# Kernel tuning notes

Measured on AMD Instinct MI355X. Metric: run time of the kernel, lower is better.

## Reference

```python
import jax, jax.numpy as jnp
import numpy as np

B, N, E, D, H, M, NH, T = 32, 128, 16256, 64, 128, 128, 256, 2

def setup_inputs() -> dict:
    key = jax.random.key(0)
    ks = jax.random.split(key, 20)
    inp = {
        'inputs': jax.random.normal(ks[0], (B, N, D), jnp.float32),
        'rel_rec': jax.random.uniform(ks[1], (E, N), jnp.float32),
        'rel_send': jax.random.uniform(ks[2], (E, N), jnp.float32),
        'rel_type': jax.random.uniform(ks[3], (B, E, T), jnp.float32),
        'indices': jnp.arange(E, dtype=jnp.int64 if jax.config.jax_enable_x64 else jnp.int32).reshape(2, E // 2),
        # per-edge-type MLP weights (torch Linear: w [out,in], b [out])
        'msg_fc1_w': jax.random.normal(ks[4], (T, H, D), jnp.float32) * 0.05,
        'msg_fc1_b': jax.random.normal(ks[5], (T, H), jnp.float32) * 0.05,
        'msg_fc2_w': jax.random.normal(ks[6], (T, M, H), jnp.float32) * 0.05,
        'msg_fc2_b': jax.random.normal(ks[7], (T, M), jnp.float32) * 0.05,
        'msg_fc3_w': jax.random.normal(ks[8], (T, H, D), jnp.float32) * 0.05,
        'msg_fc3_b': jax.random.normal(ks[9], (T, H), jnp.float32) * 0.05,
        'msg_fc4_w': jax.random.normal(ks[10], (T, M, H), jnp.float32) * 0.05,
        'msg_fc4_b': jax.random.normal(ks[11], (T, M), jnp.float32) * 0.05,
        'out_fc1_w': jax.random.normal(ks[12], (NH, M), jnp.float32) * 0.05,
        'out_fc1_b': jax.random.normal(ks[13], (NH,), jnp.float32) * 0.05,
        'out_fc2_w': jax.random.normal(ks[14], (NH, NH), jnp.float32) * 0.05,
        'out_fc2_b': jax.random.normal(ks[15], (NH,), jnp.float32) * 0.05,
        'out_fc3_w': jax.random.normal(ks[16], (D, NH), jnp.float32) * 0.05,
        'out_fc3_b': jax.random.normal(ks[17], (D,), jnp.float32) * 0.05,
    }
    return inp

def _linear(x, w, b):
    return jnp.einsum('bed,od->beo', x, w) + b

def reference(inputs, rel_rec, rel_send, rel_type, indices,
              msg_fc1_w, msg_fc1_b, msg_fc2_w, msg_fc2_b,
              msg_fc3_w, msg_fc3_b, msg_fc4_w, msg_fc4_b,
              out_fc1_w, out_fc1_b, out_fc2_w, out_fc2_b, out_fc3_w, out_fc3_b):
    # pre_msg: [B, E, D]
    pre_msg = jnp.einsum('en,bnd->bed', rel_send, inputs)
    idx_s, idx_a = indices[0], indices[1]  # disjoint edge-id partitions
    all_msgs = jnp.zeros((pre_msg.shape[0], pre_msg.shape[1], M), pre_msg.dtype)
    pm_s = pre_msg[:, idx_s, :]  # [B, E/2, D]
    pm_a = pre_msg[:, idx_a, :]
    for i in range(T):  # small fixed edge-type loop (dropout p=0 -> no-op)
        m_s = jax.nn.relu(_linear(jax.nn.relu(_linear(pm_s, msg_fc1_w[i], msg_fc1_b[i])), msg_fc2_w[i], msg_fc2_b[i]))
        m_s = m_s * rel_type[:, idx_s, i:i + 1]
        all_msgs = all_msgs.at[:, idx_s, :].add(m_s)
        m_a = jax.nn.relu(_linear(jax.nn.relu(_linear(pm_a, msg_fc3_w[i], msg_fc3_b[i])), msg_fc4_w[i], msg_fc4_b[i]))
        m_a = m_a * rel_type[:, idx_a, i:i + 1]
        all_msgs = all_msgs.at[:, idx_a, :].add(m_a)
    # aggregate: [B, N, M]
    agg = jnp.einsum('bem,en->bnm', all_msgs, rel_rec)
    h = jax.nn.relu(jnp.einsum('bnm,om->bno', agg, out_fc1_w) + out_fc1_b)
    h = jax.nn.relu(jnp.einsum('bnh,oh->bno', h, out_fc2_w) + out_fc2_b)
    pred = jnp.einsum('bnh,oh->bno', h, out_fc3_w) + out_fc3_b
    return inputs + pred
```

## Files before the change

kernel.cpp:

```cpp
#include <hip/hip_runtime.h>
#include <hip/hip_bf16.h>

#define NB 32
#define NN 128
#define NE 16256
#define ND 64
#define NHID 128
#define NM 128
#define NOH 256
#define NT 2
#define EHALF 8128
#define NTILE 127
#define TILE_E 64

typedef short s16x8 __attribute__((ext_vector_type(8)));
typedef short s16x4 __attribute__((ext_vector_type(4)));
typedef float f32x4 __attribute__((ext_vector_type(4)));

#define MFMA16(a, b, c) __builtin_amdgcn_mfma_f32_16x16x32_bf16((a), (b), (c), 0, 0, 0)

#define PARTIAL_SZ ((size_t)256 * 128 * 128 * 2)
#define WS_RS      (PARTIAL_SZ)
#define RS_SZ      ((size_t)NE * 128 * 2)
#define WS_RRT     (WS_RS + RS_SZ)
#define RRT_SZ     ((size_t)128 * NE * 2)
#define WS_IWA     (WS_RRT + RRT_SZ)
#define IWA_SZ     ((size_t)NB * 2 * 2 * 128 * 128 * 2)
#define WS_OW      (WS_IWA + IWA_SZ)
#define OW_SZ      ((size_t)(32768 + 65536 + 16384) * 2)

__device__ __forceinline__ ushort f2bf(float x) {
    uint u = __float_as_uint(x);
    return (ushort)((u + 0x7fffu + ((u >> 16) & 1u)) >> 16);
}
__device__ __forceinline__ float bf2f(ushort h) {
    return __uint_as_float(((uint)h) << 16);
}
__device__ __forceinline__ float4 ldg4(const float* p) {
    return *reinterpret_cast<const float4*>(p);
}
__device__ __forceinline__ uint cvtpk(float lo, float hi) {
    uint r;
    asm("v_cvt_pk_bf16_f32 %0, %1, %2" : "=v"(r) : "v"(lo), "v"(hi));
    return r;
}
__device__ __forceinline__ char* swz16(void* base, int row, int bir) {
    return (char*)base + row * 256 + (bir ^ ((row & 15) << 4));
}
__device__ __forceinline__ const char* swz16c(const void* base, int row, int bir) {
    return (const char*)base + row * 256 + (bir ^ ((row & 15) << 4));
}
__device__ __forceinline__ char* swz8(void* base, int row, int bir) {
    return (char*)base + row * 128 + (bir ^ ((row & 7) << 4));
}
__device__ __forceinline__ const char* swz8c(const void* base, int row, int bir) {
    return (const char*)base + row * 128 + (bir ^ ((row & 7) << 4));
}
__device__ __forceinline__ char* swzR(void* base, int row, int rowBytes, int bir) {
    return (char*)base + row * rowBytes + (bir ^ ((row & 15) << 4));
}
__device__ __forceinline__ const char* swzRc(const void* base, int row, int rowBytes, int bir) {
    return (const char*)base + row * rowBytes + (bir ^ ((row & 15) << 4));
}
__device__ __forceinline__ void gload16(const void* g, void* l) {
    __builtin_amdgcn_global_load_lds(
        (const __attribute__((address_space(1))) void*)g,
        (__attribute__((address_space(3))) void*)l, 16, 0, 0);
}

__global__ __launch_bounds__(256)
void k_pre(const float* __restrict__ inputs,
           const float* __restrict__ rel_rec, const float* __restrict__ rel_send,
           const float* __restrict__ w1, const float* __restrict__ w3,
           const float* __restrict__ ow1, const float* __restrict__ ow2,
           const float* __restrict__ ow3,
           char* __restrict__ ws)
{
    ushort* rs  = (ushort*)(ws + WS_RS);
    ushort* rrT = (ushort*)(ws + WS_RRT);
    const int t = threadIdx.x;
    const int blk = blockIdx.x;
    __shared__ float lds[128][65];

    if (blk < 127) {
        const int eb = blk;
        for (int nh = 0; nh < 2; ++nh) {
            __syncthreads();
            for (int i = t; i < 128 * 64; i += 256) {
                int e = i >> 6, n = i & 63;
                lds[e][n] = rel_rec[(size_t)(eb * 128 + e) * 128 + nh * 64 + n];
            }
            __syncthreads();
            for (int i = t; i < 64 * 128; i += 256) {
                int n = i >> 7, e = i & 127;
                rrT[(size_t)(nh * 64 + n) * NE + eb * 128 + e] = f2bf(lds[e][n]);
            }
        }
    } else if (blk < 254) {
        const int eb = blk - 127;
        const float4* src = (const float4*)(rel_send + (size_t)eb * 16384);
        for (int i = t; i < 4096; i += 256) {
            float4 v = src[i];
            ushort4 o;
            o.x = f2bf(v.x); o.y = f2bf(v.y); o.z = f2bf(v.z); o.w = f2bf(v.w);
            *(ushort4*)(rs + (size_t)eb * 16384 + (size_t)i * 4) = o;
        }
    } else if (blk < 382) {
        ushort* iwa = (ushort*)(ws + WS_IWA);
        const int wg = blk - 254;
        const int b = wg >> 2, half = (wg >> 1) & 1, it = wg & 1;
        const float* WA  = (half ? w3 : w1) + (size_t)it * NHID * ND;
        const float* inp = inputs + (size_t)b * NN * ND;
        ushort* dst = iwa + (size_t)wg * NHID * NN;

        const int lane = t & 63, wave = t >> 6;
        const int l16 = lane & 15, l4 = lane >> 4;

        for (int hh = 0; hh < 2; ++hh) {
            const int ht = wave * 2 + hh;
            s16x8 bf[2];
#pragma unroll
            for (int ks = 0; ks < 2; ++ks) {
                const float* p = WA + (size_t)(ht * 16 + l16) * ND + ks * 32 + l4 * 8;
                float4 u = ldg4(p), v = ldg4(p + 4);
                s16x8 f;
                f[0] = (short)f2bf(u.x); f[1] = (short)f2bf(u.y);
                f[2] = (short)f2bf(u.z); f[3] = (short)f2bf(u.w);
                f[4] = (short)f2bf(v.x); f[5] = (short)f2bf(v.y);
                f[6] = (short)f2bf(v.z); f[7] = (short)f2bf(v.w);
                bf[ks] = f;
            }
            for (int nt = 0; nt < 8; ++nt) {
                s16x8 af[2];
#pragma unroll
                for (int ks = 0; ks < 2; ++ks) {
                    const float* p = inp + (size_t)(nt * 16 + l16) * ND + ks * 32 + l4 * 8;
                    float4 u = ldg4(p), v = ldg4(p + 4);
                    s16x8 f;
                    f[0] = (short)f2bf(u.x); f[1] = (short)f2bf(u.y);
                    f[2] = (short)f2bf(u.z); f[3] = (short)f2bf(u.w);
                    f[4] = (short)f2bf(v.x); f[5] = (short)f2bf(v.y);
                    f[6] = (short)f2bf(v.z); f[7] = (short)f2bf(v.w);
                    af[ks] = f;
                }
                f32x4 c = (f32x4){0.f, 0.f, 0.f, 0.f};
                c = MFMA16(af[0], bf[0], c);
                c = MFMA16(af[1], bf[1], c);
                s16x4 o;
                o[0] = (short)f2bf(c[0]); o[1] = (short)f2bf(c[1]);
                o[2] = (short)f2bf(c[2]); o[3] = (short)f2bf(c[3]);
                *(s16x4*)&dst[(size_t)(ht * 16 + l16) * NN + nt * 16 + l4 * 4] = o;
            }
        }
    } else {
        ushort* owbf = (ushort*)(ws + WS_OW);
        for (int i = t; i < 4096; i += 256) {
            const int ln = i & 63, ks = (i >> 6) & 3, ot = i >> 8;
            const float* src = ow1 + (size_t)(ot * 16 + (ln & 15)) * 128 + ks * 32 + (ln >> 4) * 8;
            ushort* d = owbf + (size_t)i * 8;
#pragma unroll
            for (int j = 0; j < 8; ++j) d[j] = f2bf(src[j]);
        }
        for (int i = t; i < 8192; i += 256) {
            const int ln = i & 63, ks = (i >> 6) & 7, ot = i >> 9;
            const float* src = ow2 + (size_t)(ot * 16 + (ln & 15)) * 256 + ks * 32 + (ln >> 4) * 8;
            ushort* d = owbf + 32768 + (size_t)i * 8;
#pragma unroll
            for (int j = 0; j < 8; ++j) d[j] = f2bf(src[j]);
        }
        for (int i = t; i < 2048; i += 256) {
            const int ln = i & 63, ks = (i >> 6) & 7, dt = i >> 9;
            const float* src = ow3 + (size_t)(dt * 16 + (ln & 15)) * 256 + ks * 32 + (ln >> 4) * 8;
            ushort* d = owbf + 98304 + (size_t)i * 8;
#pragma unroll
            for (int j = 0; j < 8; ++j) d[j] = f2bf(src[j]);
        }
    }
}

__global__ __launch_bounds__(512, 1)
void k_edge(const float* __restrict__ rel_type,
            const float* __restrict__ b1, const float* __restrict__ b2,
            const float* __restrict__ b3, const float* __restrict__ b4,
            const float* __restrict__ w2, const float* __restrict__ w4,
            char* __restrict__ ws)
{
    const ushort* rsg = (const ushort*)(ws + WS_RS);
    const ushort* rrT = (const ushort*)(ws + WS_RRT);
    const ushort* iwa = (const ushort*)(ws + WS_IWA);
    ushort* partial   = (ushort*)ws;

    const int tid  = threadIdx.x;
    const int wave = tid >> 6;
    const int lane = tid & 63;
    const int l16  = lane & 15;
    const int l4   = lane >> 4;

    const int wg    = blockIdx.x;
    const int b     = wg >> 3;
    const int half  = (wg >> 2) & 1;
    const int chunk = wg & 3;

    const float* BA    = half ? b3 : b1;
    const float* BB    = half ? b4 : b2;
    const float* WBsrc = half ? w4 : w2;

    __shared__ ushort H_s[2][2][64 * 128];
    __shared__ ushort rs_s[2][64 * 128];
    __shared__ ushort rr_s[2][128 * 64];
    __shared__ ushort Mt_s[128 * 64];
    __shared__ float  rt_s[2][128];

    s16x8 wIW[2][4];
    const ushort* iwb = iwa + (size_t)((b * 2 + half) * 2) * NHID * NN;
#pragma unroll
    for (int it = 0; it < 2; ++it)
#pragma unroll
        for (int ks = 0; ks < 4; ++ks)
            wIW[it][ks] = *(const s16x8*)(iwb + (size_t)it * NHID * NN +
                                          (size_t)(wave * 16 + l16) * NN + ks * 32 + l4 * 8);
    s16x8 wB[2][4];
#pragma unroll
    for (int it = 0; it < 2; ++it)
#pragma unroll
        for (int ks = 0; ks < 4; ++ks) {
            const float* p = WBsrc + (size_t)(it * NM + wave * 16 + l16) * NHID + ks * 32 + l4 * 8;
            float4 u = ldg4(p), v = ldg4(p + 4);
            s16x8 f;
            f[0] = (short)f2bf(u.x); f[1] = (short)f2bf(u.y);
            f[2] = (short)f2bf(u.z); f[3] = (short)f2bf(u.w);
            f[4] = (short)f2bf(v.x); f[5] = (short)f2bf(v.y);
            f[6] = (short)f2bf(v.z); f[7] = (short)f2bf(v.w);
            wB[it][ks] = f;
        }
    float biasA[2] = {BA[wave * 16 + l16], BA[NHID + wave * 16 + l16]};
    float biasB[2] = {BB[wave * 16 + l16], BB[NM + wave * 16 + l16]};

    f32x4 agg[8];
#pragma unroll
    for (int r = 0; r < 8; ++r) agg[r] = (f32x4){0.f, 0.f, 0.f, 0.f};

    const int t0 = chunk * 32;
    const int t1 = (t0 + 32 < NTILE) ? (t0 + 32) : NTILE;

    {
        const int ebase0 = half * EHALF + t0 * TILE_E;
#pragma unroll
        for (int s = 0; s < 2; ++s) {
            const int i = s * 512 + tid;
            const int e = i >> 4, c = i & 15;
            const int cp = c ^ (e & 15);
            gload16(rsg + (size_t)(ebase0 + e) * 128 + cp * 8, (char*)&rs_s[0][0] + i * 16);
        }
    }
    __syncthreads();

    for (int t = t0; t < t1; ++t) {
        const int buf  = (t - t0) & 1;
        const int nbuf = buf ^ 1;
        const int ebase = half * EHALF + t * TILE_E;
        const bool do_next = (t + 1) < t1;

#pragma unroll
        for (int s = 0; s < 2; ++s) {
            const int j = s * 512 + tid;
            const int n = j >> 3, c = j & 7;
            const int cp = c ^ (n & 7);
            gload16(rrT + (size_t)n * NE + ebase + cp * 8, (char*)&rr_s[buf][0] + j * 16);
        }
        if (do_next) {
            const int ebn = ebase + TILE_E;
#pragma unroll
            for (int s = 0; s < 2; ++s) {
                const int i = s * 512 + tid;
                const int e = i >> 4, c = i & 15;
                const int cp = c ^ (e & 15);
                gload16(rsg + (size_t)(ebn + e) * 128 + cp * 8, (char*)&rs_s[nbuf][0] + i * 16);
            }
        }
        if (tid < 128)
            rt_s[buf][tid] = rel_type[((size_t)b * NE + ebase + (tid >> 1)) * NT + (tid & 1)];

#pragma unroll
        for (int et = 0; et < 4; ++et) {
            const int erow = et * 16 + l16;
            s16x8 a0 = *(const s16x8*)swz16c(&rs_s[buf][0], erow, 0 * 64 + l4 * 16);
            s16x8 a1 = *(const s16x8*)swz16c(&rs_s[buf][0], erow, 1 * 64 + l4 * 16);
            s16x8 a2 = *(const s16x8*)swz16c(&rs_s[buf][0], erow, 2 * 64 + l4 * 16);
            s16x8 a3 = *(const s16x8*)swz16c(&rs_s[buf][0], erow, 3 * 64 + l4 * 16);
#pragma unroll
            for (int it = 0; it < 2; ++it) {
                f32x4 c = (f32x4){0.f, 0.f, 0.f, 0.f};
                __builtin_amdgcn_s_setprio(1);
                c = MFMA16(a0, wIW[it][0], c);
                c = MFMA16(a1, wIW[it][1], c);
                c = MFMA16(a2, wIW[it][2], c);
                c = MFMA16(a3, wIW[it][3], c);
                __builtin_amdgcn_s_setprio(0);
#pragma unroll
                for (int r = 0; r < 4; ++r) {
                    const int er = et * 16 + l4 * 4 + r;
                    *(ushort*)swz16(&H_s[buf][it][0], er, (wave * 16 + l16) * 2) =
                        f2bf(fmaxf(c[r] + biasA[it], 0.f));
                }
            }
        }
        __syncthreads();

        float macc[4][4];
#pragma unroll
        for (int et = 0; et < 4; ++et)
#pragma unroll
            for (int r = 0; r < 4; ++r) macc[et][r] = 0.f;

#pragma unroll
        for (int et = 0; et < 4; ++et) {
            const int e = et * 16 + l16;
            float2 rtv[4];
#pragma unroll
            for (int r = 0; r < 4; ++r)
                rtv[r] = *(const float2*)&rt_s[buf][(et * 16 + l4 * 4 + r) * 2];
#pragma unroll
            for (int it = 0; it < 2; ++it) {
                f32x4 c = (f32x4){0.f, 0.f, 0.f, 0.f};
                __builtin_amdgcn_s_setprio(1);
#pragma unroll
                for (int ks = 0; ks < 4; ++ks) {
                    s16x8 a = *(const s16x8*)swz16c(&H_s[buf][it][0], e, ks * 64 + l4 * 16);
                    c = MFMA16(a, wB[it][ks], c);
                }
                __builtin_amdgcn_s_setprio(0);
#pragma unroll
                for (int r = 0; r < 4; ++r)
                    macc[et][r] += fmaxf(c[r] + biasB[it], 0.f) * (it ? rtv[r].y : rtv[r].x);
            }
        }

        {
            const int m = wave * 16 + l16;
#pragma unroll
            for (int et = 0; et < 4; ++et) {
                uint2 v;
                v.x = cvtpk(macc[et][0], macc[et][1]);
                v.y = cvtpk(macc[et][2], macc[et][3]);
                *(uint2*)swz8(Mt_s, m, et * 32 + l4 * 8) = v;
            }
            s16x8 bb0 = *(const s16x8*)swz8c(Mt_s, m, 0 * 64 + l4 * 16);
            s16x8 bb1 = *(const s16x8*)swz8c(Mt_s, m, 1 * 64 + l4 * 16);
            __builtin_amdgcn_s_setprio(1);
#pragma unroll
            for (int nt = 0; nt < 8; ++nt) {
                const int n = nt * 16 + l16;
                s16x8 a0 = *(const s16x8*)swz8c(&rr_s[buf][0], n, 0 * 64 + l4 * 16);
                s16x8 a1 = *(const s16x8*)swz8c(&rr_s[buf][0], n, 1 * 64 + l4 * 16);
                agg[nt] = MFMA16(a0, bb0, agg[nt]);
                agg[nt] = MFMA16(a1, bb1, agg[nt]);
            }
            __builtin_amdgcn_s_setprio(0);
        }
    }

    {
        ushort* dst = partial + (size_t)wg * (NN * NM);
        const int m = wave * 16 + l16;
#pragma unroll
        for (int nt = 0; nt < 8; ++nt) {
            uint2 v;
            v.x = cvtpk(agg[nt][0], agg[nt][1]);
            v.y = cvtpk(agg[nt][2], agg[nt][3]);
            *(uint2*)&dst[(size_t)m * NN + nt * 16 + l4 * 4] = v;
        }
    }
}

__global__ __launch_bounds__(512)
void k_out(const ushort* __restrict__ partial,
           const ushort* __restrict__ owbf,
           const float* __restrict__ inputs,
           const float* __restrict__ ob1, const float* __restrict__ ob2,
           const float* __restrict__ ob3,
           float* __restrict__ out)
{
    const int t    = threadIdx.x;
    const int wave = t >> 6;
    const int lane = t & 63;
    const int l16  = lane & 15;
    const int l4   = lane >> 4;
    const int wg   = blockIdx.x;
    const int b    = wg >> 3;
    const int n0   = (wg & 7) * 16;

    __shared__ ushort xA[16 * 128];
    __shared__ ushort h1A[16 * 256];
    __shared__ ushort h2A[16 * 256];

    {
        const int m = t >> 2, g = t & 3;
        float s0 = 0.f, s1 = 0.f, s2 = 0.f, s3 = 0.f;
#pragma unroll
        for (int c = 0; c < 8; ++c) {
            const ushort* p = partial + ((size_t)(b * 8 + c)) * (NN * NM) +
                              (size_t)m * NN + n0 + g * 4;
            s16x4 v = *(const s16x4*)p;
            s0 += bf2f((ushort)v[0]); s1 += bf2f((ushort)v[1]);
            s2 += bf2f((ushort)v[2]); s3 += bf2f((ushort)v[3]);
        }
        *(ushort*)swzR(xA, g * 4 + 0, 256, m * 2) = f2bf(s0);
        *(ushort*)swzR(xA, g * 4 + 1, 256, m * 2) = f2bf(s1);
        *(ushort*)swzR(xA, g * 4 + 2, 256, m * 2) = f2bf(s2);
        *(ushort*)swzR(xA, g * 4 + 3, 256, m * 2) = f2bf(s3);
    }
    __syncthreads();

    {
        s16x8 ka[4];
#pragma unroll
        for (int ks = 0; ks < 4; ++ks)
            ka[ks] = *(const s16x8*)swzRc(xA, l16, 256, ks * 64 + l4 * 16);
#pragma unroll
        for (int ot = 0; ot < 2; ++ot) {
            const int otg = wave * 2 + ot;
            const int o = otg * 16 + l16;
            f32x4 c = (f32x4){0.f, 0.f, 0.f, 0.f};
#pragma unroll
            for (int ks = 0; ks < 4; ++ks) {
                s16x8 wb = *(const s16x8*)&owbf[((size_t)(otg * 4 + ks) * 64 + lane) * 8];
                c = MFMA16(ka[ks], wb, c);
            }
            const float bias = ob1[o];
#pragma unroll
            for (int r = 0; r < 4; ++r)
                *(ushort*)swzR(h1A, l4 * 4 + r, 512, o * 2) =
                    f2bf(fmaxf(c[r] + bias, 0.f));
        }
    }
    __syncthreads();

    {
        s16x8 ka[8];
#pragma unroll
        for (int ks = 0; ks < 8; ++ks)
            ka[ks] = *(const s16x8*)swzRc(h1A, l16, 512, ks * 64 + l4 * 16);
        const ushort* w2f = owbf + 32768;
#pragma unroll
        for (int ot = 0; ot < 2; ++ot) {
            const int otg = wave * 2 + ot;
            const int o = otg * 16 + l16;
            f32x4 c = (f32x4){0.f, 0.f, 0.f, 0.f};
#pragma unroll
            for (int ks = 0; ks < 8; ++ks) {
                s16x8 wb = *(const s16x8*)&w2f[((size_t)(otg * 8 + ks) * 64 + lane) * 8];
                c = MFMA16(ka[ks], wb, c);
            }
            const float bias = ob2[o];
#pragma unroll
            for (int r = 0; r < 4; ++r)
                *(ushort*)swzR(h2A, l4 * 4 + r, 512, o * 2) =
                    f2bf(fmaxf(c[r] + bias, 0.f));
        }
    }
    __syncthreads();

    if (wave < 4) {
        s16x8 ka[8];
#pragma unroll
        for (int ks = 0; ks < 8; ++ks)
            ka[ks] = *(const s16x8*)swzRc(h2A, l16, 512, ks * 64 + l4 * 16);
        const ushort* w3f = owbf + 98304;
        const int d = wave * 16 + l16;
        f32x4 c = (f32x4){0.f, 0.f, 0.f, 0.f};
#pragma unroll
        for (int ks = 0; ks < 8; ++ks) {
            s16x8 wb = *(const s16x8*)&w3f[((size_t)(wave * 8 + ks) * 64 + lane) * 8];
            c = MFMA16(ka[ks], wb, c);
        }
        const float bias = ob3[d];
#pragma unroll
        for (int r = 0; r < 4; ++r) {
            const int n = n0 + l4 * 4 + r;
            const size_t idx = ((size_t)b * NN + n) * ND + d;
            out[idx] = inputs[idx] + c[r] + bias;
        }
    }
}

extern "C" void kernel_launch(void* const* d_in, const int* in_sizes, int n_in,
                              void* d_out, int out_size, void* d_ws, size_t ws_size,
                              hipStream_t stream)
{
    const float* inputs   = (const float*)d_in[0];
    const float* rel_rec  = (const float*)d_in[1];
    const float* rel_send = (const float*)d_in[2];
    const float* rel_type = (const float*)d_in[3];
    const float* w1  = (const float*)d_in[5];
    const float* b1  = (const float*)d_in[6];
    const float* w2  = (const float*)d_in[7];
    const float* b2  = (const float*)d_in[8];
    const float* w3  = (const float*)d_in[9];
    const float* b3  = (const float*)d_in[10];
    const float* w4  = (const float*)d_in[11];
    const float* b4  = (const float*)d_in[12];
    const float* ow1 = (const float*)d_in[13];
    const float* ob1 = (const float*)d_in[14];
    const float* ow2 = (const float*)d_in[15];
    const float* ob2 = (const float*)d_in[16];
    const float* ow3 = (const float*)d_in[17];
    const float* ob3 = (const float*)d_in[18];

    char* ws = (char*)d_ws;

    k_pre <<<dim3(383), dim3(256), 0, stream>>>(inputs, rel_rec, rel_send,
                                                w1, w3, ow1, ow2, ow3, ws);
    k_edge<<<dim3(256), dim3(512), 0, stream>>>(rel_type,
                                                b1, b2, b3, b4, w2, w4, ws);
    k_out <<<dim3(256), dim3(512), 0, stream>>>((const ushort*)ws,
                                                (const ushort*)(ws + WS_OW),
                                                inputs, ob1, ob2, ob3,
                                                (float*)d_out);
}
```

Baseline: 156.2 us.

## Re-split edge-MLP work across waves by edge type and tile aggregation GEMM

The edge kernel now assigns each wave a single edge type (wi) and a 32-column slice, in place of every wave handling both types for a 16-column slice. H fragments are loaded from LDS once and reused across both output tiles. Per-type messages go to separate Mt buffers, and the aggregation GEMM uses a 2x4 register tile per wave, so rr_s and Mt_s fragments are reused across several MFMAs. The pre-kernel swaps scalar bf16 rounding for packed v_cvt_pk conversions and transposes rel_rec through a bf16 LDS tile with vectorized 16-byte stores. The change adds an extra __syncthreads per tile and alters the accumulation order: the two edge types are now summed in fp32 MFMA accumulators after separate bf16 rounding.

```diff
diff --git a/kernel.cpp b/kernel.cpp
--- a/kernel.cpp
+++ b/kernel.cpp
@@ -43,6 +43,17 @@
     uint r;
     asm("v_cvt_pk_bf16_f32 %0, %1, %2" : "=v"(r) : "v"(lo), "v"(hi));
     return r;
+}
+__device__ __forceinline__ ushort f2bf1(float x) {
+    return (ushort)cvtpk(x, 0.f);
+}
+__device__ __forceinline__ s16x8 pack8(float4 u, float4 v) {
+    uint4 o;
+    o.x = cvtpk(u.x, u.y);
+    o.y = cvtpk(u.z, u.w);
+    o.z = cvtpk(v.x, v.y);
+    o.w = cvtpk(v.z, v.w);
+    return *(s16x8*)&o;
 }
 __device__ __forceinline__ char* swz16(void* base, int row, int bir) {
     return (char*)base + row * 256 + (bir ^ ((row & 15) << 4));
@@ -80,30 +91,36 @@
     ushort* rrT = (ushort*)(ws + WS_RRT);
     const int t = threadIdx.x;
     const int blk = blockIdx.x;
-    __shared__ float lds[128][65];
 
     if (blk < 127) {
+        __shared__ ushort tl[128][130];
         const int eb = blk;
-        for (int nh = 0; nh < 2; ++nh) {
-            __syncthreads();
-            for (int i = t; i < 128 * 64; i += 256) {
-                int e = i >> 6, n = i & 63;
-                lds[e][n] = rel_rec[(size_t)(eb * 128 + e) * 128 + nh * 64 + n];
-            }
-            __syncthreads();
-            for (int i = t; i < 64 * 128; i += 256) {
-                int n = i >> 7, e = i & 127;
-                rrT[(size_t)(nh * 64 + n) * NE + eb * 128 + e] = f2bf(lds[e][n]);
-            }
+        for (int i = t; i < 4096; i += 256) {
+            const int e = i >> 5, nq = i & 31;
+            float4 v = ldg4(rel_rec + (size_t)(eb * 128 + e) * 128 + nq * 4);
+            uint2 o;
+            o.x = cvtpk(v.x, v.y);
+            o.y = cvtpk(v.z, v.w);
+            *(uint2*)&tl[e][nq * 4] = o;
+        }
+        __syncthreads();
+        const int n = t >> 1, part = t & 1;
+        for (int c = 0; c < 8; ++c) {
+            const int e0 = part * 64 + c * 8;
+            s16x8 v;
+#pragma unroll
+            for (int j = 0; j < 8; ++j) v[j] = (short)tl[e0 + j][n];
+            *(s16x8*)&rrT[(size_t)n * NE + eb * 128 + e0] = v;
         }
     } else if (blk < 254) {
         const int eb = blk - 127;
         const float4* src = (const float4*)(rel_send + (size_t)eb * 16384);
         for (int i = t; i < 4096; i += 256) {
             float4 v = src[i];
-            ushort4 o;
-            o.x = f2bf(v.x); o.y = f2bf(v.y); o.z = f2bf(v.z); o.w = f2bf(v.w);
-            *(ushort4*)(rs + (size_t)eb * 16384 + (size_t)i * 4) = o;
+            uint2 o;
+            o.x = cvtpk(v.x, v.y);
+            o.y = cvtpk(v.z, v.w);
+            *(uint2*)(rs + (size_t)eb * 16384 + (size_t)i * 4) = o;
         }
     } else if (blk < 382) {
         ushort* iwa = (ushort*)(ws + WS_IWA);
@@ -122,34 +139,22 @@
 #pragma unroll
             for (int ks = 0; ks < 2; ++ks) {
                 const float* p = WA + (size_t)(ht * 16 + l16) * ND + ks * 32 + l4 * 8;
-                float4 u = ldg4(p), v = ldg4(p + 4);
-                s16x8 f;
-                f[0] = (short)f2bf(u.x); f[1] = (short)f2bf(u.y);
-                f[2] = (short)f2bf(u.z); f[3] = (short)f2bf(u.w);
-                f[4] = (short)f2bf(v.x); f[5] = (short)f2bf(v.y);
-                f[6] = (short)f2bf(v.z); f[7] = (short)f2bf(v.w);
-                bf[ks] = f;
+                bf[ks] = pack8(ldg4(p), ldg4(p + 4));
             }
             for (int nt = 0; nt < 8; ++nt) {
                 s16x8 af[2];
 #pragma unroll
                 for (int ks = 0; ks < 2; ++ks) {
                     const float* p = inp + (size_t)(nt * 16 + l16) * ND + ks * 32 + l4 * 8;
-                    float4 u = ldg4(p), v = ldg4(p + 4);
-                    s16x8 f;
-                    f[0] = (short)f2bf(u.x); f[1] = (short)f2bf(u.y);
-                    f[2] = (short)f2bf(u.z); f[3] = (short)f2bf(u.w);
-                    f[4] = (short)f2bf(v.x); f[5] = (short)f2bf(v.y);
-                    f[6] = (short)f2bf(v.z); f[7] = (short)f2bf(v.w);
-                    af[ks] = f;
+                    af[ks] = pack8(ldg4(p), ldg4(p + 4));
                 }
                 f32x4 c = (f32x4){0.f, 0.f, 0.f, 0.f};
                 c = MFMA16(af[0], bf[0], c);
                 c = MFMA16(af[1], bf[1], c);
-                s16x4 o;
-                o[0] = (short)f2bf(c[0]); o[1] = (short)f2bf(c[1]);
-                o[2] = (short)f2bf(c[2]); o[3] = (short)f2bf(c[3]);
-                *(s16x4*)&dst[(size_t)(ht * 16 + l16) * NN + nt * 16 + l4 * 4] = o;
+                uint2 o;
+                o.x = cvtpk(c[0], c[1]);
+                o.y = cvtpk(c[2], c[3]);
+                *(uint2*)&dst[(size_t)(ht * 16 + l16) * NN + nt * 16 + l4 * 4] = o;
             }
         }
     } else {
@@ -195,6 +200,10 @@
     const int lane = tid & 63;
     const int l16  = lane & 15;
     const int l4   = lane >> 4;
+    const int wi   = wave & 1;
+    const int wg2  = wave >> 1;
+    const int wn   = wave & 3;
+    const int wm2  = wave >> 2;
 
     const int wg    = blockIdx.x;
     const int b     = wg >> 3;
@@ -205,40 +214,43 @@
     const float* BB    = half ? b4 : b2;
     const float* WBsrc = half ? w4 : w2;
 
-    __shared__ ushort H_s[2][2][64 * 128];
+    __shared__ ushort H_s[2][64 * 128];
     __shared__ ushort rs_s[2][64 * 128];
     __shared__ ushort rr_s[2][128 * 64];
-    __shared__ ushort Mt_s[128 * 64];
+    __shared__ ushort Mt_s[2][128 * 64];
     __shared__ float  rt_s[2][128];
 
     s16x8 wIW[2][4];
-    const ushort* iwb = iwa + (size_t)((b * 2 + half) * 2) * NHID * NN;
-#pragma unroll
-    for (int it = 0; it < 2; ++it)
-#pragma unroll
-        for (int ks = 0; ks < 4; ++ks)
-            wIW[it][ks] = *(const s16x8*)(iwb + (size_t)it * NHID * NN +
-                                          (size_t)(wave * 16 + l16) * NN + ks * 32 + l4 * 8);
+    {
+        const ushort* iwb = iwa + (size_t)((b * 2 + half) * 2 + wi) * NHID * NN;
+#pragma unroll
+        for (int ht = 0; ht < 2; ++ht)
+#pragma unroll
+            for (int ks = 0; ks < 4; ++ks)
+                wIW[ht][ks] = *(const s16x8*)(iwb +
+                    (size_t)(wg2 * 32 + ht * 16 + l16) * NN + ks * 32 + l4 * 8);
+    }
     s16x8 wB[2][4];
 #pragma unroll
-    for (int it = 0; it < 2; ++it)
+    for (int mt = 0; mt < 2; ++mt)
 #pragma unroll
         for (int ks = 0; ks < 4; ++ks) {
-            const float* p = WBsrc + (size_t)(it * NM + wave * 16 + l16) * NHID + ks * 32 + l4 * 8;
-            float4 u = ldg4(p), v = ldg4(p + 4);
-            s16x8 f;
-            f[0] = (short)f2bf(u.x); f[1] = (short)f2bf(u.y);
-            f[2] = (short)f2bf(u.z); f[3] = (short)f2bf(u.w);
-            f[4] = (short)f2bf(v.x); f[5] = (short)f2bf(v.y);
-            f[6] = (short)f2bf(v.z); f[7] = (short)f2bf(v.w);
-            wB[it][ks] = f;
-        }
-    float biasA[2] = {BA[wave * 16 + l16], BA[NHID + wave * 16 + l16]};
-    float biasB[2] = {BB[wave * 16 + l16], BB[NM + wave * 16 + l16]};
-
-    f32x4 agg[8];
-#pragma unroll
-    for (int r = 0; r < 8; ++r) agg[r] = (f32x4){0.f, 0.f, 0.f, 0.f};
+            const float* p = WBsrc +
+                (size_t)(wi * NM + wg2 * 32 + mt * 16 + l16) * NHID + ks * 32 + l4 * 8;
+            wB[mt][ks] = pack8(ldg4(p), ldg4(p + 4));
+        }
+    float biasA[2], biasB[2];
+#pragma unroll
+    for (int q = 0; q < 2; ++q) {
+        biasA[q] = BA[wi * NHID + wg2 * 32 + q * 16 + l16];
+        biasB[q] = BB[wi * NM + wg2 * 32 + q * 16 + l16];
+    }
+
+    f32x4 agg[2][4];
+#pragma unroll
+    for (int i = 0; i < 2; ++i)
+#pragma unroll
+        for (int j = 0; j < 4; ++j) agg[i][j] = (f32x4){0.f, 0.f, 0.f, 0.f};
 
     const int t0 = chunk * 32;
     const int t1 = (t0 + 32 < NTILE) ? (t0 + 32) : NTILE;
@@ -289,87 +301,88 @@
             s16x8 a2 = *(const s16x8*)swz16c(&rs_s[buf][0], erow, 2 * 64 + l4 * 16);
             s16x8 a3 = *(const s16x8*)swz16c(&rs_s[buf][0], erow, 3 * 64 + l4 * 16);
 #pragma unroll
-            for (int it = 0; it < 2; ++it) {
+            for (int ht = 0; ht < 2; ++ht) {
                 f32x4 c = (f32x4){0.f, 0.f, 0.f, 0.f};
                 __builtin_amdgcn_s_setprio(1);
-                c = MFMA16(a0, wIW[it][0], c);
-                c = MFMA16(a1, wIW[it][1], c);
-                c = MFMA16(a2, wIW[it][2], c);
-                c = MFMA16(a3, wIW[it][3], c);
+                c = MFMA16(a0, wIW[ht][0], c);
+                c = MFMA16(a1, wIW[ht][1], c);
+                c = MFMA16(a2, wIW[ht][2], c);
+                c = MFMA16(a3, wIW[ht][3], c);
                 __builtin_amdgcn_s_setprio(0);
+                const int hcol = wg2 * 32 + ht * 16 + l16;
 #pragma unroll
                 for (int r = 0; r < 4; ++r) {
                     const int er = et * 16 + l4 * 4 + r;
-                    *(ushort*)swz16(&H_s[buf][it][0], er, (wave * 16 + l16) * 2) =
-                        f2bf(fmaxf(c[r] + biasA[it], 0.f));
+                    *(ushort*)swz16(&H_s[wi][0], er, hcol * 2) =
+                        f2bf1(fmaxf(c[r] + biasA[ht], 0.f));
                 }
             }
         }
         __syncthreads();
-
-        float macc[4][4];
-#pragma unroll
-        for (int et = 0; et < 4; ++et)
-#pragma unroll
-            for (int r = 0; r < 4; ++r) macc[et][r] = 0.f;
 
 #pragma unroll
         for (int et = 0; et < 4; ++et) {
             const int e = et * 16 + l16;
-            float2 rtv[4];
+            s16x8 a0 = *(const s16x8*)swz16c(&H_s[wi][0], e, 0 * 64 + l4 * 16);
+            s16x8 a1 = *(const s16x8*)swz16c(&H_s[wi][0], e, 1 * 64 + l4 * 16);
+            s16x8 a2 = *(const s16x8*)swz16c(&H_s[wi][0], e, 2 * 64 + l4 * 16);
+            s16x8 a3 = *(const s16x8*)swz16c(&H_s[wi][0], e, 3 * 64 + l4 * 16);
+            float rtv[4];
 #pragma unroll
             for (int r = 0; r < 4; ++r)
-                rtv[r] = *(const float2*)&rt_s[buf][(et * 16 + l4 * 4 + r) * 2];
-#pragma unroll
-            for (int it = 0; it < 2; ++it) {
+                rtv[r] = rt_s[buf][(et * 16 + l4 * 4 + r) * 2 + wi];
+#pragma unroll
+            for (int mt = 0; mt < 2; ++mt) {
                 f32x4 c = (f32x4){0.f, 0.f, 0.f, 0.f};
                 __builtin_amdgcn_s_setprio(1);
-#pragma unroll
-                for (int ks = 0; ks < 4; ++ks) {
-                    s16x8 a = *(const s16x8*)swz16c(&H_s[buf][it][0], e, ks * 64 + l4 * 16);
-                    c = MFMA16(a, wB[it][ks], c);
+                c = MFMA16(a0, wB[mt][0], c);
+                c = MFMA16(a1, wB[mt][1], c);
+                c = MFMA16(a2, wB[mt][2], c);
+                c = MFMA16(a3, wB[mt][3], c);
+                __builtin_amdgcn_s_setprio(0);
+                const int m = wg2 * 32 + mt * 16 + l16;
+                uint2 v;
+                v.x = cvtpk(fmaxf(c[0] + biasB[mt], 0.f) * rtv[0],
+                            fmaxf(c[1] + biasB[mt], 0.f) * rtv[1]);
+                v.y = cvtpk(fmaxf(c[2] + biasB[mt], 0.f) * rtv[2],
+                            fmaxf(c[3] + biasB[mt], 0.f) * rtv[3]);
+                *(uint2*)swz8(&Mt_s[wi][0], m, et * 32 + l4 * 8) = v;
+            }
+        }
+        __syncthreads();
+
+#pragma unroll
+        for (int ks = 0; ks < 2; ++ks) {
+            s16x8 aa0 = *(const s16x8*)swz8c(&rr_s[buf][0], wn * 32 + 0 * 16 + l16, ks * 64 + l4 * 16);
+            s16x8 aa1 = *(const s16x8*)swz8c(&rr_s[buf][0], wn * 32 + 1 * 16 + l16, ks * 64 + l4 * 16);
+#pragma unroll
+            for (int it = 0; it < 2; ++it) {
+                __builtin_amdgcn_s_setprio(1);
+#pragma unroll
+                for (int mt = 0; mt < 4; ++mt) {
+                    s16x8 bb = *(const s16x8*)swz8c(&Mt_s[it][0],
+                        wm2 * 64 + mt * 16 + l16, ks * 64 + l4 * 16);
+                    agg[0][mt] = MFMA16(aa0, bb, agg[0][mt]);
+                    agg[1][mt] = MFMA16(aa1, bb, agg[1][mt]);
                 }
                 __builtin_amdgcn_s_setprio(0);
-#pragma unroll
-                for (int r = 0; r < 4; ++r)
-                    macc[et][r] += fmaxf(c[r] + biasB[it], 0.f) * (it ? rtv[r].y : rtv[r].x);
-            }
-        }
-
-        {
-            const int m = wave * 16 + l16;
-#pragma unroll
-            for (int et = 0; et < 4; ++et) {
-                uint2 v;
-                v.x = cvtpk(macc[et][0], macc[et][1]);
-                v.y = cvtpk(macc[et][2], macc[et][3]);
-                *(uint2*)swz8(Mt_s, m, et * 32 + l4 * 8) = v;
-            }
-            s16x8 bb0 = *(const s16x8*)swz8c(Mt_s, m, 0 * 64 + l4 * 16);
-            s16x8 bb1 = *(const s16x8*)swz8c(Mt_s, m, 1 * 64 + l4 * 16);
-            __builtin_amdgcn_s_setprio(1);
-#pragma unroll
-            for (int nt = 0; nt < 8; ++nt) {
-                const int n = nt * 16 + l16;
-                s16x8 a0 = *(const s16x8*)swz8c(&rr_s[buf][0], n, 0 * 64 + l4 * 16);
-                s16x8 a1 = *(const s16x8*)swz8c(&rr_s[buf][0], n, 1 * 64 + l4 * 16);
-                agg[nt] = MFMA16(a0, bb0, agg[nt]);
-                agg[nt] = MFMA16(a1, bb1, agg[nt]);
-            }
-            __builtin_amdgcn_s_setprio(0);
+            }
         }
     }
 
     {
         ushort* dst = partial + (size_t)wg * (NN * NM);
-        const int m = wave * 16 + l16;
-#pragma unroll
-        for (int nt = 0; nt < 8; ++nt) {
-            uint2 v;
-            v.x = cvtpk(agg[nt][0], agg[nt][1]);
-            v.y = cvtpk(agg[nt][2], agg[nt][3]);
-            *(uint2*)&dst[(size_t)m * NN + nt * 16 + l4 * 4] = v;
-        }
+#pragma unroll
+        for (int nt = 0; nt < 2; ++nt)
+#pragma unroll
+            for (int mt = 0; mt < 4; ++mt) {
+                const int m  = wm2 * 64 + mt * 16 + l16;
+                const int n0 = wn * 32 + nt * 16 + l4 * 4;
+                uint2 v;
+                v.x = cvtpk(agg[nt][mt][0], agg[nt][mt][1]);
+                v.y = cvtpk(agg[nt][mt][2], agg[nt][mt][3]);
+                *(uint2*)&dst[(size_t)m * NN + n0] = v;
+            }
     }
 }
 
```

New measurement: 160.0 us. +2.4%, slower.
